# Optimization experiments

Hardware: AMD Instinct MI355X
Metric: run time of the kernel (lower is better)

The kernel has to match this reference:

```python
import jax, jax.numpy as jnp
import numpy as np

# Fixed architecture constants (match init_kwargs)
D_MODEL = 256
NHEAD = 8
BASE_WINDOW = 4
DFF = 1024
B = 1
S = 4096


def _win_idx(grid, w):
    """Token indices of overlapping w x w windows over a grid x grid image,
    stride w//2 (same windows as F.unfold(kernel=w, stride=w//2)). -> (L, w*w) int32."""
    s = w // 2
    starts = np.arange(0, grid - w + 1, s)
    rows = starts[:, None] + np.arange(w)[None, :]              # (n, w)
    idx = rows[:, None, :, None] * grid + rows[None, :, None, :]  # (n, n, w, w)
    return jnp.asarray(idx.reshape(-1, w * w), dtype=jnp.int32)


def _ln(x, g, b, eps=1e-5):
    m = jnp.mean(x, axis=-1, keepdims=True)
    v = jnp.var(x, axis=-1, keepdims=True)
    return (x - m) * jax.lax.rsqrt(v + eps) * g + b


def _local_attn(x, scale, fw, fb, fg, fbb):
    """Multi-scale windowed SDPA: gather windows, attend, mean-pool per window,
    scatter pooled features back to token positions (overlap-averaged), fuse."""
    Bq, Sq, Dm = x.shape
    grid = int(np.sqrt(Sq))
    inv_scale = 1.0 / float(np.sqrt(Dm))  # SDPA uses full D as head dim
    outs = []
    for i in range(3):
        w = BASE_WINDOW * (2 ** i) * scale
        idx = _win_idx(grid, w)                      # (L, w2)
        win = x[:, idx, :]                           # (B, L, w2, D) gather
        p = jax.nn.softmax(jnp.einsum('blqd,blkd->blqk', win, win) * inv_scale, axis=-1)
        pooled = jnp.einsum('blqk,blkd->blqd', p, win).mean(axis=2)  # (B, L, D)
        flat = idx.reshape(-1)
        contrib = jnp.broadcast_to(pooled[:, :, None, :], win.shape).reshape(Bq, -1, Dm)
        acc = jnp.zeros_like(x).at[:, flat, :].add(contrib)
        cnt = jnp.zeros((Sq,), x.dtype).at[flat].add(1.0)
        outs.append(acc / cnt[None, :, None])        # (B, S, D) per scale
    cat = jnp.concatenate(outs, axis=-1)             # (B, S, 3D)
    return _ln(cat @ fw + fb, fg, fbb)


def _mha(x, wq, wk, wv, bq, bk, bv, wo, bo):
    Bq, Sq, Dm = x.shape
    dh = Dm // NHEAD
    def split(t):
        return t.reshape(Bq, Sq, NHEAD, dh)
    q, k, v = split(x @ wq + bq), split(x @ wk + bk), split(x @ wv + bv)
    p = jax.nn.softmax(jnp.einsum('bqhd,bkhd->bhqk', q, k) * (1.0 / float(np.sqrt(dh))), axis=-1)
    o = jnp.einsum('bhqk,bkhd->bqhd', p, v).reshape(Bq, Sq, Dm)
    return o @ wo + bo


def _forward(x, pos, fw, fb, fg, fbb, wq, wk, wv, bq, bk, bv, wo, bo, gw, gb, w1, b1, w2, b2, n1g, n1b, n2g, n2b, n3g, n3b, local_scale):
    # pos is accepted but unused in the original math (device check only)
    xl = _local_attn(x, local_scale, fw, fb, fg, fbb)
    xl = _ln(x + xl, n1g, n1b)                 # norm1 residual (dropout is identity in eval)
    xg = _mha(xl, wq, wk, wv, bq, bk, bv, wo, bo)
    xg = _ln(xl + xg, n2g, n2b)                # norm2 residual
    gate = jax.nn.softmax(((xl + xg) * 0.5).mean(axis=1, keepdims=True) @ gw + gb, axis=-1)  # (B,1,2)
    alpha, beta = gate[..., 0:1], gate[..., 1:2]
    xf = alpha * xg + beta * xl
    ff = jax.nn.gelu(xf @ w1 + b1, approximate=False) @ w2 + b2
    return _ln(xf + ff, n3g, n3b)


def setup_inputs() -> dict:
    key = jax.random.key(0)
    ks = jax.random.split(key, 12)
    def rn(k, shape, s=0.02):
        return jax.random.normal(k, shape, jnp.float32) * s
    D = D_MODEL
    return {
        'x': jax.random.normal(ks[0], (B, S, D), jnp.float32),
        'pos': jax.random.normal(ks[1], (B, S, 2), jnp.float32),
        'fw': rn(ks[2], (3 * D, D)), 'fb': jnp.zeros((D,), jnp.float32),
        'fg': jnp.ones((D,), jnp.float32), 'fbb': jnp.zeros((D,), jnp.float32),
        'wq': rn(ks[3], (D, D)), 'wk': rn(ks[4], (D, D)), 'wv': rn(ks[5], (D, D)),
        'bq': jnp.zeros((D,), jnp.float32), 'bk': jnp.zeros((D,), jnp.float32), 'bv': jnp.zeros((D,), jnp.float32),
        'wo': rn(ks[6], (D, D)), 'bo': jnp.zeros((D,), jnp.float32),
        'gw': rn(ks[7], (D, 2)), 'gb': jnp.zeros((2,), jnp.float32),
        'w1': rn(ks[8], (D, DFF)), 'b1': jnp.zeros((DFF,), jnp.float32),
        'w2': rn(ks[9], (DFF, D)), 'b2': jnp.zeros((D,), jnp.float32),
        'n1g': jnp.ones((D,), jnp.float32), 'n1b': jnp.zeros((D,), jnp.float32),
        'n2g': jnp.ones((D,), jnp.float32), 'n2b': jnp.zeros((D,), jnp.float32),
        'n3g': jnp.ones((D,), jnp.float32), 'n3b': jnp.zeros((D,), jnp.float32),
        'local_scale': 1,
    }


def reference(x, pos, fw, fb, fg, fbb, wq, wk, wv, bq, bk, bv, wo, bo, gw, gb, w1, b1, w2, b2, n1g, n1b, n2g, n2b, n3g, n3b, local_scale):
    return _forward(x, pos, fw, fb, fg, fbb, wq, wk, wv, bq, bk, bv, wo, bo, gw, gb, w1, b1, w2, b2, n1g, n1b, n2g, n2b, n3g, n3b, local_scale)
```

## Files before the change

### kernel.cpp

```cpp
#include <hip/hip_runtime.h>
#include <hip/hip_bf16.h>
#include <cstdint>
#include <cstddef>


#define DEVFN __device__ __forceinline__

constexpr int S    = 4096;
constexpr int D    = 256;
constexpr int GRID = 64;
constexpr int NH   = 8;
constexpr int DH   = 32;

typedef __attribute__((ext_vector_type(8))) short bf16x8;
typedef __attribute__((ext_vector_type(4))) float f32x4;
typedef __attribute__((ext_vector_type(16))) float f32x16;
typedef __attribute__((ext_vector_type(2))) unsigned int u32x2;

DEVFN float asf(unsigned u) { return __uint_as_float(u); }

DEVFN unsigned short f2bf(float f) {
  unsigned u = __float_as_uint(f);
  u += 0x7fffu + ((u >> 16) & 1u);
  return (unsigned short)(u >> 16);
}
DEVFN float bf2f(unsigned short s) { return __uint_as_float(((unsigned)s) << 16); }

DEVFN unsigned pk2(float a, float b) {
  __hip_bfloat162 h = __float22bfloat162_rn(make_float2(a, b));
  return *(unsigned*)&h;
}

DEVFN bf16x8 pack8(float4 a, float4 b) {
  union { unsigned w[4]; bf16x8 v; } u;
  u.w[0] = pk2(a.x, a.y); u.w[1] = pk2(a.z, a.w);
  u.w[2] = pk2(b.x, b.y); u.w[3] = pk2(b.z, b.w);
  return u.v;
}

DEVFN float ex2(float x) {
#if __has_builtin(__builtin_amdgcn_exp2f)
  return __builtin_amdgcn_exp2f(x);
#else
  return __expf(x * 0.6931471805599453f);
#endif
}

DEVFN float gelu_t(float u) {
  const float y = 0.7978845608028654f * (u + 0.044715f * u * u * u);
  const float e = __expf(2.f * y);
  return 0.5f * u * (2.f - 2.f / (e + 1.f));
}

__global__ __launch_bounds__(256) void k_wt(
    const float* fw, const float* wq, const float* wk, const float* wv,
    const float* wo, const float* w1, const float* w2,
    unsigned short* fwT, unsigned short* wqT, unsigned short* wkT,
    unsigned short* wvT, unsigned short* woT, unsigned short* w1T,
    unsigned short* w2T) {
  __shared__ unsigned short tile[32][36];
  const int bid = blockIdx.x;
  const float* src; unsigned short* dst; int K, N, t;
  if (bid < 192)      { src = fw; dst = fwT; K = 768;  N = 256;  t = bid; }
  else if (bid < 256) { src = wq; dst = wqT; K = 256;  N = 256;  t = bid - 192; }
  else if (bid < 320) { src = wk; dst = wkT; K = 256;  N = 256;  t = bid - 256; }
  else if (bid < 384) { src = wv; dst = wvT; K = 256;  N = 256;  t = bid - 320; }
  else if (bid < 448) { src = wo; dst = woT; K = 256;  N = 256;  t = bid - 384; }
  else if (bid < 704) { src = w1; dst = w1T; K = 256;  N = 1024; t = bid - 448; }
  else                { src = w2; dst = w2T; K = 1024; N = 256;  t = bid - 704; }
  const int nkt = K >> 5;
  const int k0 = (t % nkt) * 32, n0 = (t / nkt) * 32;
  const int i = threadIdx.x >> 3, j4 = threadIdx.x & 7;
  const float4 v = *(const float4*)(src + (size_t)(k0 + i) * N + n0 + j4 * 4);
  *(uint2*)&tile[i][j4 * 4] = make_uint2(pk2(v.x, v.y), pk2(v.z, v.w));
  __syncthreads();
  unsigned o0 = tile[j4 * 4 + 0][i], o1 = tile[j4 * 4 + 1][i];
  unsigned o2 = tile[j4 * 4 + 2][i], o3 = tile[j4 * 4 + 3][i];
  *(uint2*)(dst + (size_t)(n0 + i) * K + k0 + j4 * 4) =
      make_uint2(o0 | (o1 << 16), o2 | (o3 << 16));
}

template <int K, int OUTBF, int ACT>
__global__ __launch_bounds__(64) void k_gemm_m(const unsigned short* __restrict__ Ab,
                                               const unsigned short* __restrict__ WT,
                                               const float* __restrict__ bias,
                                               void* __restrict__ Cout, int N) {
  const int lane = threadIdx.x;
  const int lc = lane & 31, hi = lane >> 5;
  const int m0 = blockIdx.x * 32, n0 = blockIdx.y * 32;
  const unsigned short* ap = Ab + (size_t)(m0 + lc) * K + hi * 8;
  const unsigned short* bp = WT + (size_t)(n0 + lc) * K + hi * 8;
  f32x16 acc0 = {0.f,0.f,0.f,0.f,0.f,0.f,0.f,0.f,0.f,0.f,0.f,0.f,0.f,0.f,0.f,0.f};
  f32x16 acc1 = acc0;
#pragma unroll 8
  for (int k0 = 0; k0 < K; k0 += 32) {
    bf16x8 a0 = *(const bf16x8*)(ap + k0);
    bf16x8 b0 = *(const bf16x8*)(bp + k0);
    bf16x8 a1 = *(const bf16x8*)(ap + k0 + 16);
    bf16x8 b1 = *(const bf16x8*)(bp + k0 + 16);
    acc0 = __builtin_amdgcn_mfma_f32_32x32x16_bf16(a0, b0, acc0, 0, 0, 0);
    acc1 = __builtin_amdgcn_mfma_f32_32x32x16_bf16(a1, b1, acc1, 0, 0, 0);
  }
  const float bv = bias[n0 + lc];
#pragma unroll
  for (int r = 0; r < 16; ++r) {
    const int row = (r & 3) + 8 * (r >> 2) + 4 * hi;
    float v = acc0[r] + acc1[r] + bv;
    if (ACT == 1) v = gelu_t(v);
    if (OUTBF) ((unsigned short*)Cout)[(size_t)(m0 + row) * N + n0 + lc] = f2bf(v);
    else       ((float*)Cout)[(size_t)(m0 + row) * N + n0 + lc] = v;
  }
}

__global__ __launch_bounds__(64) void k_gemm_qkv(const unsigned short* __restrict__ Ab,
                                                 const unsigned short* __restrict__ wqkvT,
                                                 const float* __restrict__ bq,
                                                 const float* __restrict__ bk,
                                                 const float* __restrict__ bv,
                                                 unsigned short* __restrict__ qb,
                                                 unsigned short* __restrict__ kb,
                                                 unsigned short* __restrict__ vb) {
  const int lane = threadIdx.x;
  const int lc = lane & 31, hi = lane >> 5;
  const int m0 = blockIdx.x * 32;
  const int sel = blockIdx.y >> 3, n0 = (blockIdx.y & 7) * 32;
  const unsigned short* WT = wqkvT + (size_t)sel * 256 * 256;
  const float* bias = sel == 0 ? bq : sel == 1 ? bk : bv;
  unsigned short* out = sel == 0 ? qb : sel == 1 ? kb : vb;
  const float oscale = sel == 0 ? 0.25505889254f : 1.f;
  const unsigned short* ap = Ab + (size_t)(m0 + lc) * 256 + hi * 8;
  const unsigned short* bp = WT + (size_t)(n0 + lc) * 256 + hi * 8;
  f32x16 acc0 = {0.f,0.f,0.f,0.f,0.f,0.f,0.f,0.f,0.f,0.f,0.f,0.f,0.f,0.f,0.f,0.f};
  f32x16 acc1 = acc0;
#pragma unroll 8
  for (int k0 = 0; k0 < 256; k0 += 32) {
    bf16x8 a0 = *(const bf16x8*)(ap + k0);
    bf16x8 b0 = *(const bf16x8*)(bp + k0);
    bf16x8 a1 = *(const bf16x8*)(ap + k0 + 16);
    bf16x8 b1 = *(const bf16x8*)(bp + k0 + 16);
    acc0 = __builtin_amdgcn_mfma_f32_32x32x16_bf16(a0, b0, acc0, 0, 0, 0);
    acc1 = __builtin_amdgcn_mfma_f32_32x32x16_bf16(a1, b1, acc1, 0, 0, 0);
  }
  const float bvv = bias[n0 + lc];
#pragma unroll
  for (int r = 0; r < 16; ++r) {
    const int row = (r & 3) + 8 * (r >> 2) + 4 * hi;
    out[(size_t)(m0 + row) * 256 + n0 + lc] = f2bf((acc0[r] + acc1[r] + bvv) * oscale);
  }
}

template <int W, int THREADS>
__global__ __launch_bounds__(THREADS) void k_local_s(const float* __restrict__ x,
                                                     float* __restrict__ pooled, int nS) {
  constexpr int NT  = W * W;
  constexpr int NCT = NT / 16;
  constexpr int LDE = 264;
  __shared__ unsigned short win[NT][LDE];
  __shared__ float a[NT];
  const int tid = threadIdx.x;
  const int wave = tid >> 6, lane = tid & 63;
  const int lr = lane & 15, lg = lane >> 4;
  const int l = blockIdx.x;
  const int row0 = (l / nS) * (W / 2), col0 = (l % nS) * (W / 2);

  for (int e8 = tid; e8 < NT * 32; e8 += THREADS) {
    const int t = e8 >> 5, c8 = (e8 & 31) * 8;
    const float* src = x + ((size_t)((row0 + t / W) * GRID + col0 + (t % W))) * D + c8;
    *(bf16x8*)&win[t][c8] = pack8(*(const float4*)src, *(const float4*)(src + 4));
  }
  if (tid < NT) a[tid] = 0.f;
  __syncthreads();

  bf16x8 af[8];
#pragma unroll
  for (int k2 = 0; k2 < 8; ++k2)
    af[k2] = *(const bf16x8*)&win[wave * 16 + lr][k2 * 32 + lg * 8];

  float m[4], Z[4], Zi[4];
#pragma unroll
  for (int r = 0; r < 4; ++r) { m[r] = -INFINITY; Z[r] = 0.f; }

  for (int ct = 0; ct < NCT; ++ct) {
    f32x4 Ca = {0.f, 0.f, 0.f, 0.f}, Cb = {0.f, 0.f, 0.f, 0.f};
#pragma unroll
    for (int k2 = 0; k2 < 8; k2 += 2) {
      bf16x8 b0 = *(const bf16x8*)&win[ct * 16 + lr][k2 * 32 + lg * 8];
      bf16x8 b1 = *(const bf16x8*)&win[ct * 16 + lr][(k2 + 1) * 32 + lg * 8];
      Ca = __builtin_amdgcn_mfma_f32_16x16x32_bf16(af[k2], b0, Ca, 0, 0, 0);
      Cb = __builtin_amdgcn_mfma_f32_16x16x32_bf16(af[k2 + 1], b1, Cb, 0, 0, 0);
    }
#pragma unroll
    for (int r = 0; r < 4; ++r) {
      const float sv = (Ca[r] + Cb[r]) * 0.0625f;
      const float nm = fmaxf(m[r], sv);
      Z[r] = Z[r] * __expf(m[r] - nm) + __expf(sv - nm);
      m[r] = nm;
    }
  }
#pragma unroll
  for (int r = 0; r < 4; ++r) {
#pragma unroll
    for (int msk = 1; msk <= 8; msk <<= 1) {
      const float om = __shfl_xor(m[r], msk), oz = __shfl_xor(Z[r], msk);
      const float nm = fmaxf(m[r], om);
      Z[r] = Z[r] * __expf(m[r] - nm) + oz * __expf(om - nm);
      m[r] = nm;
    }
    Zi[r] = 1.f / Z[r];
  }

  for (int ct = 0; ct < NCT; ++ct) {
    f32x4 Ca = {0.f, 0.f, 0.f, 0.f}, Cb = {0.f, 0.f, 0.f, 0.f};
#pragma unroll
    for (int k2 = 0; k2 < 8; k2 += 2) {
      bf16x8 b0 = *(const bf16x8*)&win[ct * 16 + lr][k2 * 32 + lg * 8];
      bf16x8 b1 = *(const bf16x8*)&win[ct * 16 + lr][(k2 + 1) * 32 + lg * 8];
      Ca = __builtin_amdgcn_mfma_f32_16x16x32_bf16(af[k2], b0, Ca, 0, 0, 0);
      Cb = __builtin_amdgcn_mfma_f32_16x16x32_bf16(af[k2 + 1], b1, Cb, 0, 0, 0);
    }
    float cs = 0.f;
#pragma unroll
    for (int r = 0; r < 4; ++r)
      cs += __expf((Ca[r] + Cb[r]) * 0.0625f - m[r]) * Zi[r];
    cs += __shfl_xor(cs, 16);
    cs += __shfl_xor(cs, 32);
    if (lg == 0) atomicAdd(&a[ct * 16 + lr], cs);
  }
  __syncthreads();

  for (int d = tid; d < D; d += THREADS) {
    float acc = 0.f;
#pragma unroll 8
    for (int k = 0; k < NT; ++k) acc += a[k] * bf2f(win[k][d]);
    pooled[(size_t)l * D + d] = acc * (1.f / NT);
  }
}

__global__ __launch_bounds__(256, 1) void k_local16(const float* __restrict__ x,
                                                    float* __restrict__ pooled, int nS) {
  constexpr int LDE = 264;
  __shared__ unsigned short win[256][LDE];
  __shared__ float a[256];
  const int tid = threadIdx.x;
  const int wave = tid >> 6, lane = tid & 63;
  const int lc = lane & 31, hi = lane >> 5;
  const int l = blockIdx.x, z = blockIdx.y;
  const int row0 = (l / nS) * 8, col0 = (l % nS) * 8;

  for (int e8 = tid; e8 < 256 * 32; e8 += 256) {
    const int t = e8 >> 5, c8 = (e8 & 31) * 8;
    const float* src = x + ((size_t)((row0 + (t >> 4)) * GRID + col0 + (t & 15))) * D + c8;
    *(bf16x8*)&win[t][c8] = pack8(*(const float4*)src, *(const float4*)(src + 4));
  }
  a[tid] = 0.f;
  __syncthreads();

  const int R0 = (z * 4 + wave) * 32;
  bf16x8 af[16];
#pragma unroll
  for (int k2 = 0; k2 < 16; ++k2)
    af[k2] = *(const bf16x8*)&win[R0 + lc][k2 * 16 + hi * 8];

  float m[16], Z[16], Zi[16];
#pragma unroll
  for (int r = 0; r < 16; ++r) { m[r] = -INFINITY; Z[r] = 0.f; }

  for (int ct = 0; ct < 8; ++ct) {
    f32x16 Ca = {0.f,0.f,0.f,0.f,0.f,0.f,0.f,0.f,0.f,0.f,0.f,0.f,0.f,0.f,0.f,0.f};
    f32x16 Cb = Ca;
#pragma unroll
    for (int k2 = 0; k2 < 16; k2 += 2) {
      bf16x8 b0 = *(const bf16x8*)&win[ct * 32 + lc][k2 * 16 + hi * 8];
      bf16x8 b1 = *(const bf16x8*)&win[ct * 32 + lc][(k2 + 1) * 16 + hi * 8];
      Ca = __builtin_amdgcn_mfma_f32_32x32x16_bf16(af[k2], b0, Ca, 0, 0, 0);
      Cb = __builtin_amdgcn_mfma_f32_32x32x16_bf16(af[k2 + 1], b1, Cb, 0, 0, 0);
    }
#pragma unroll
    for (int r = 0; r < 16; ++r) {
      const float sv = (Ca[r] + Cb[r]) * 0.0625f;
      const float nm = fmaxf(m[r], sv);
      Z[r] = Z[r] * __expf(m[r] - nm) + __expf(sv - nm);
      m[r] = nm;
    }
  }
#pragma unroll
  for (int r = 0; r < 16; ++r) {
#pragma unroll
    for (int msk = 1; msk <= 16; msk <<= 1) {
      const float om = __shfl_xor(m[r], msk), oz = __shfl_xor(Z[r], msk);
      const float nm = fmaxf(m[r], om);
      Z[r] = Z[r] * __expf(m[r] - nm) + oz * __expf(om - nm);
      m[r] = nm;
    }
    Zi[r] = 1.f / Z[r];
  }

  for (int ct = 0; ct < 8; ++ct) {
    f32x16 Ca = {0.f,0.f,0.f,0.f,0.f,0.f,0.f,0.f,0.f,0.f,0.f,0.f,0.f,0.f,0.f,0.f};
    f32x16 Cb = Ca;
#pragma unroll
    for (int k2 = 0; k2 < 16; k2 += 2) {
      bf16x8 b0 = *(const bf16x8*)&win[ct * 32 + lc][k2 * 16 + hi * 8];
      bf16x8 b1 = *(const bf16x8*)&win[ct * 32 + lc][(k2 + 1) * 16 + hi * 8];
      Ca = __builtin_amdgcn_mfma_f32_32x32x16_bf16(af[k2], b0, Ca, 0, 0, 0);
      Cb = __builtin_amdgcn_mfma_f32_32x32x16_bf16(af[k2 + 1], b1, Cb, 0, 0, 0);
    }
    float cs = 0.f;
#pragma unroll
    for (int r = 0; r < 16; ++r)
      cs += __expf((Ca[r] + Cb[r]) * 0.0625f - m[r]) * Zi[r];
    cs += __shfl_xor(cs, 32);
    if (hi == 0) atomicAdd(&a[ct * 32 + lc], cs);
  }
  __syncthreads();

  {
    const int d = tid;
    float acc = 0.f;
#pragma unroll 8
    for (int k = 0; k < 256; ++k) acc += a[k] * bf2f(win[k][d]);
    atomicAdd(&pooled[(size_t)l * D + d], acc * (1.f / 256.f));
  }
}

DEVFN float gatherp(const float* __restrict__ pooled, int r, int c, int W, int s, int nS, int d) {
  int amin = max(0, (r - W + s) / s), amax = min(nS - 1, r / s);
  int bmin = max(0, (c - W + s) / s), bmax = min(nS - 1, c / s);
  float acc = 0.f;
  int cnt = 0;
  for (int a = amin; a <= amax; ++a)
    for (int b = bmin; b <= bmax; ++b) { acc += pooled[(size_t)(a * nS + b) * D + d]; ++cnt; }
  return acc / (float)cnt;
}

__global__ void k_combine(const float* __restrict__ p0, const float* __restrict__ p1,
                          const float* __restrict__ p2, unsigned short* __restrict__ catb) {
  const int t = blockIdx.x, d = threadIdx.x;
  const int r = t >> 6, c = t & 63;
  unsigned short* o = catb + (size_t)t * 768;
  o[d]       = f2bf(gatherp(p0, r, c, 4, 2, 31, d));
  o[256 + d] = f2bf(gatherp(p1, r, c, 8, 4, 15, d));
  o[512 + d] = f2bf(gatherp(p2, r, c, 16, 8, 7, d));
}

DEVFN float2 block_sum2(float a, float b) {
  __shared__ float sb[8];
#pragma unroll
  for (int m = 32; m; m >>= 1) { a += __shfl_xor(a, m); b += __shfl_xor(b, m); }
  const int w = threadIdx.x >> 6;
  __syncthreads();
  if ((threadIdx.x & 63) == 0) { sb[w] = a; sb[4 + w] = b; }
  __syncthreads();
  return make_float2(sb[0] + sb[1] + sb[2] + sb[3], sb[4] + sb[5] + sb[6] + sb[7]);
}

__global__ __launch_bounds__(256) void k_ln(float* __restrict__ out, unsigned short* __restrict__ outb,
                                            const float* __restrict__ a, const float* __restrict__ b,
                                            const float* __restrict__ g, const float* __restrict__ be) {
  const size_t i = (size_t)blockIdx.x * D + threadIdx.x;
  float v = a[i] + (b ? b[i] : 0.f);
  float2 s = block_sum2(v, v * v);
  float mean = s.x * (1.f / D);
  float var = s.y * (1.f / D) - mean * mean;
  const float r = (v - mean) * rsqrtf(var + 1e-5f) * g[threadIdx.x] + be[threadIdx.x];
  out[i] = r;
  if (outb) outb[i] = f2bf(r);
}

__global__ __launch_bounds__(256) void k_ln_fuse(const float* __restrict__ t1,
                                                 const float* __restrict__ x,
                                                 float* __restrict__ xl,
                                                 unsigned short* __restrict__ xlb,
                                                 const float* __restrict__ fg,
                                                 const float* __restrict__ fbb,
                                                 const float* __restrict__ n1g,
                                                 const float* __restrict__ n1b) {
  const size_t i = (size_t)blockIdx.x * D + threadIdx.x;
  const float v1 = t1[i];
  float2 s1 = block_sum2(v1, v1 * v1);
  const float mean1 = s1.x * (1.f / D);
  const float var1 = s1.y * (1.f / D) - mean1 * mean1;
  const float r1 = (v1 - mean1) * rsqrtf(var1 + 1e-5f) * fg[threadIdx.x] + fbb[threadIdx.x];
  const float v2 = x[i] + r1;
  float2 s2 = block_sum2(v2, v2 * v2);
  const float mean2 = s2.x * (1.f / D);
  const float var2 = s2.y * (1.f / D) - mean2 * mean2;
  const float r2 = (v2 - mean2) * rsqrtf(var2 + 1e-5f) * n1g[threadIdx.x] + n1b[threadIdx.x];
  xl[i] = r2;
  xlb[i] = f2bf(r2);
}

__global__ __launch_bounds__(256) void k_flash_mfma(const unsigned short* __restrict__ Qg,
                                                    const unsigned short* __restrict__ Kg,
                                                    const unsigned short* __restrict__ Vg,
                                                    unsigned short* __restrict__ po,
                                                    float* __restrict__ pml) {
  const int h = blockIdx.y, z = blockIdx.z;
  const int tid = threadIdx.x;
  const int wave = tid >> 6, lane = tid & 63;
  const int lr = lane & 15, lg = lane >> 4;
  constexpr int NT2 = 16;

  __shared__ unsigned short Kf[2][64][40];
  __shared__ unsigned short VS[2][2048];

  const int q0 = blockIdx.x * 64 + wave * 16;
  const int kbase = z * 1024;

  const bf16x8 qfrag = *(const bf16x8*)(Qg + (size_t)(q0 + lr) * D + h * DH + lg * 8);

  f32x4 o0 = {0.f, 0.f, 0.f, 0.f}, o1 = {0.f, 0.f, 0.f, 0.f};
  float mrow = -INFINITY, lrow = 0.f;

  const unsigned vsbase0 =
      (unsigned)(unsigned long long)(const void*)&VS[0][0] + (unsigned)(lg * 128 + lr * 2);

  const int key = tid >> 2, c8 = (tid & 3) * 8;
  const int vidx = (c8 >> 4) * 1024 + (key >> 2) * 64 + (key & 3) * 16 + (c8 & 15);
  const unsigned short* kp = Kg + (size_t)(kbase + key) * D + h * DH + c8;
  const unsigned short* vp = Vg + (size_t)(kbase + key) * D + h * DH + c8;
  constexpr int KSTEP = 64 * D;

  {
    bf16x8 k0r = *(const bf16x8*)kp;
    bf16x8 v0r = *(const bf16x8*)vp;
    *(bf16x8*)&Kf[0][key][c8] = k0r;
    *(bf16x8*)&VS[0][vidx] = v0r;
  }
  __syncthreads();

  for (int kt = 0; kt < NT2; ++kt) {
    const int cur = kt & 1;
    const int ktn = (kt + 1 < NT2) ? kt + 1 : kt;
    bf16x8 kreg = *(const bf16x8*)(kp + (size_t)ktn * KSTEP);
    bf16x8 vreg = *(const bf16x8*)(vp + (size_t)ktn * KSTEP);

    f32x4 s[4];
    __builtin_amdgcn_s_setprio(1);
#pragma unroll
    for (int k16 = 0; k16 < 4; ++k16) {
      bf16x8 ka = *(const bf16x8*)&Kf[cur][k16 * 16 + lr][lg * 8];
      f32x4 zc = {0.f, 0.f, 0.f, 0.f};
      s[k16] = __builtin_amdgcn_mfma_f32_16x16x32_bf16(ka, qfrag, zc, 0, 0, 0);
    }
    __builtin_amdgcn_s_setprio(0);

    const unsigned vb = vsbase0 + (unsigned)(cur << 12);
    u32x2 tv000, tv001, tv010, tv011, tv100, tv101, tv110, tv111;
    asm volatile("ds_read_b64_tr_b16 %0, %1 offset:0"    : "=v"(tv000) : "v"(vb));
    asm volatile("ds_read_b64_tr_b16 %0, %1 offset:2048" : "=v"(tv001) : "v"(vb));
    asm volatile("ds_read_b64_tr_b16 %0, %1 offset:512"  : "=v"(tv010) : "v"(vb));
    asm volatile("ds_read_b64_tr_b16 %0, %1 offset:2560" : "=v"(tv011) : "v"(vb));
    asm volatile("ds_read_b64_tr_b16 %0, %1 offset:1024" : "=v"(tv100) : "v"(vb));
    asm volatile("ds_read_b64_tr_b16 %0, %1 offset:3072" : "=v"(tv101) : "v"(vb));
    asm volatile("ds_read_b64_tr_b16 %0, %1 offset:1536" : "=v"(tv110) : "v"(vb));
    asm volatile("ds_read_b64_tr_b16 %0, %1 offset:3584" : "=v"(tv111) : "v"(vb));

    float tm = fmaxf(fmaxf(fmaxf(s[0][0], s[0][1]), fmaxf(s[0][2], s[0][3])),
                     fmaxf(fmaxf(s[1][0], s[1][1]), fmaxf(s[1][2], s[1][3])));
    tm = fmaxf(tm, fmaxf(fmaxf(fmaxf(s[2][0], s[2][1]), fmaxf(s[2][2], s[2][3])),
                         fmaxf(fmaxf(s[3][0], s[3][1]), fmaxf(s[3][2], s[3][3]))));
    const bool skip = __all(tm - mrow <= 11.f);
    if (!skip) {
      float tmm = fmaxf(tm, __shfl_xor(tm, 16));
      tmm = fmaxf(tmm, __shfl_xor(tmm, 32));
      const float nm = fmaxf(mrow, tmm);
      const float cfac = ex2(mrow - nm);
      mrow = nm;
      lrow *= cfac;
#pragma unroll
      for (int r = 0; r < 4; ++r) {
        const float cr = __shfl(cfac, lg * 4 + r);
        o0[r] *= cr; o1[r] *= cr;
      }
    }
#pragma unroll
    for (int k16 = 0; k16 < 4; ++k16)
#pragma unroll
      for (int r = 0; r < 4; ++r) { s[k16][r] = ex2(s[k16][r] - mrow); lrow += s[k16][r]; }

    asm volatile("s_waitcnt lgkmcnt(0)" ::: "memory");
    __builtin_amdgcn_sched_barrier(0);

    union VB { u32x2 u2[2]; bf16x8 b; };
    __builtin_amdgcn_s_setprio(1);
#pragma unroll
    for (int kt2 = 0; kt2 < 2; ++kt2) {
      union { unsigned w[4]; bf16x8 v; } pu;
      pu.w[0] = pk2(s[2 * kt2][0], s[2 * kt2][1]);
      pu.w[1] = pk2(s[2 * kt2][2], s[2 * kt2][3]);
      pu.w[2] = pk2(s[2 * kt2 + 1][0], s[2 * kt2 + 1][1]);
      pu.w[3] = pk2(s[2 * kt2 + 1][2], s[2 * kt2 + 1][3]);
      VB v0f, v1f;
      if (kt2 == 0) { v0f.u2[0] = tv000; v0f.u2[1] = tv010; v1f.u2[0] = tv001; v1f.u2[1] = tv011; }
      else          { v0f.u2[0] = tv100; v0f.u2[1] = tv110; v1f.u2[0] = tv101; v1f.u2[1] = tv111; }
      o0 = __builtin_amdgcn_mfma_f32_16x16x32_bf16(pu.v, v0f.b, o0, 0, 0, 0);
      o1 = __builtin_amdgcn_mfma_f32_16x16x32_bf16(pu.v, v1f.b, o1, 0, 0, 0);
    }
    __builtin_amdgcn_s_setprio(0);

    if (kt + 1 < NT2) {
      *(bf16x8*)&Kf[cur ^ 1][key][c8] = kreg;
      *(bf16x8*)&VS[cur ^ 1][vidx] = vreg;
      __syncthreads();
    }
  }

  lrow += __shfl_xor(lrow, 16);
  lrow += __shfl_xor(lrow, 32);

#pragma unroll
  for (int r = 0; r < 4; ++r) {
    unsigned short* op = po + (size_t)z * S * D + (size_t)(q0 + lg * 4 + r) * D + h * DH + lr;
    op[0]  = f2bf(o0[r]);
    op[16] = f2bf(o1[r]);
  }
  if (lane < 16) {
    float* mlp = pml + ((size_t)(z * NH + h) * S + q0 + lr) * 2;
    mlp[0] = mrow;
    mlp[1] = lrow;
  }
}

__global__ __launch_bounds__(256) void k_fmerge(const unsigned short* __restrict__ po,
                                                const float* __restrict__ pml,
                                                unsigned short* __restrict__ t1b) {
  const int t = blockIdx.x, d = threadIdx.x;
  const int h = d >> 5;
  float m[4], l[4];
  float M = -INFINITY;
#pragma unroll
  for (int z = 0; z < 4; ++z) {
    const float* ml = pml + ((size_t)(z * NH + h) * S + t) * 2;
    m[z] = ml[0]; l[z] = ml[1];
    M = fmaxf(M, m[z]);
  }
  float L = 0.f, acc = 0.f;
#pragma unroll
  for (int z = 0; z < 4; ++z) {
    const float a = ex2(m[z] - M);
    L += l[z] * a;
    acc += bf2f(po[(size_t)z * S * D + (size_t)t * D + d]) * a;
  }
  t1b[(size_t)t * D + d] = f2bf(acc / L);
}

__global__ __launch_bounds__(256) void k_colmean(const float* __restrict__ xl,
                                                 const float* __restrict__ xg,
                                                 float* __restrict__ gbuf) {
  const int j = threadIdx.x;
  const int t0 = blockIdx.x * 64;
  float s = 0.f;
  for (int t = 0; t < 64; ++t) {
    size_t i = (size_t)(t0 + t) * D + j;
    s += xl[i] + xg[i];
  }
  atomicAdd(&gbuf[j], s * 0.5f);
}

__global__ __launch_bounds__(256) void k_gate(float* __restrict__ gbuf,
                                              const float* __restrict__ gw,
                                              const float* __restrict__ gb) {
  const int j = threadIdx.x;
  const float gm = gbuf[j] * (1.f / (float)S);
  float2 s = block_sum2(gm * gw[2 * j], gm * gw[2 * j + 1]);
  if (j == 0) {
    float g0 = s.x + gb[0], g1 = s.y + gb[1];
    float mx = fmaxf(g0, g1);
    float e0 = __expf(g0 - mx), e1 = __expf(g1 - mx);
    gbuf[256] = e0 / (e0 + e1);
    gbuf[257] = e1 / (e0 + e1);
  }
}

__global__ __launch_bounds__(256) void k_xf(const float* __restrict__ xl,
                                            const float* __restrict__ xg,
                                            const float* __restrict__ gbuf,
                                            float* __restrict__ xf,
                                            unsigned short* __restrict__ xfb) {
  const float alpha = gbuf[256], beta = gbuf[257];
  const size_t i = ((size_t)blockIdx.x * 256 + threadIdx.x) * 4;
  float4 a = *(const float4*)(xg + i);
  float4 b = *(const float4*)(xl + i);
  float4 r;
  r.x = alpha * a.x + beta * b.x;
  r.y = alpha * a.y + beta * b.y;
  r.z = alpha * a.z + beta * b.z;
  r.w = alpha * a.w + beta * b.w;
  *(float4*)(xf + i) = r;
  *(uint2*)(xfb + i) = make_uint2(pk2(r.x, r.y), pk2(r.z, r.w));
}

extern "C" void kernel_launch(void* const* d_in, const int* in_sizes, int n_in,
                              void* d_out, int out_size, void* d_ws, size_t ws_size,
                              hipStream_t stream) {
  const float* x   = (const float*)d_in[0];
  const float* fw  = (const float*)d_in[2];
  const float* fb  = (const float*)d_in[3];
  const float* fg  = (const float*)d_in[4];
  const float* fbb = (const float*)d_in[5];
  const float* wq  = (const float*)d_in[6];
  const float* wk  = (const float*)d_in[7];
  const float* wv  = (const float*)d_in[8];
  const float* bq  = (const float*)d_in[9];
  const float* bk  = (const float*)d_in[10];
  const float* bv  = (const float*)d_in[11];
  const float* wo  = (const float*)d_in[12];
  const float* bo  = (const float*)d_in[13];
  const float* gw  = (const float*)d_in[14];
  const float* gb  = (const float*)d_in[15];
  const float* w1  = (const float*)d_in[16];
  const float* b1  = (const float*)d_in[17];
  const float* w2  = (const float*)d_in[18];
  const float* b2  = (const float*)d_in[19];
  const float* n1g = (const float*)d_in[20];
  const float* n1b = (const float*)d_in[21];
  const float* n2g = (const float*)d_in[22];
  const float* n2b = (const float*)d_in[23];
  const float* n3g = (const float*)d_in[24];
  const float* n3b = (const float*)d_in[25];
  float* out = (float*)d_out;

  char* base = (char*)d_ws;
  size_t off = 0;
  auto carve = [&](size_t bytes) { char* p = base + off; off += (bytes + 255) & ~(size_t)255; return p; };
  float* p0 = (float*)carve(961 * 256 * 4);
  float* p1 = (float*)carve(225 * 256 * 4);
  float* p2 = (float*)carve(49 * 256 * 4);
  unsigned short* fwT = (unsigned short*)carve(256 * 768 * 2);
  unsigned short* wqkvT = (unsigned short*)carve(3 * 256 * 256 * 2);
  unsigned short* wqT = wqkvT;
  unsigned short* wkT = wqkvT + 256 * 256;
  unsigned short* wvT = wqkvT + 2 * 256 * 256;
  unsigned short* woT = (unsigned short*)carve(256 * 256 * 2);
  unsigned short* w1T = (unsigned short*)carve(1024 * 256 * 2);
  unsigned short* w2T = (unsigned short*)carve(256 * 1024 * 2);
  char* R = carve(8388608);
  unsigned short* catb = (unsigned short*)R;
  unsigned short* po   = (unsigned short*)R;
  float* xg            = (float*)R;
  unsigned short* hbuf = (unsigned short*)R;
  float* pml = (float*)carve(4 * NH * (size_t)S * 2 * 4);
  unsigned short* qb = (unsigned short*)carve((size_t)S * D * 2);
  unsigned short* kb = (unsigned short*)carve((size_t)S * D * 2);
  unsigned short* vb = (unsigned short*)carve((size_t)S * D * 2);
  float* xf            = (float*)qb;
  unsigned short* xfb  = vb;
  float* t1  = (float*)carve((size_t)S * D * 4);
  float* ffo = t1;
  unsigned short* t1b = (unsigned short*)carve((size_t)S * D * 2);
  float* xl  = (float*)carve((size_t)S * D * 4);
  unsigned short* xlb = (unsigned short*)carve((size_t)S * D * 2);
  float* gbuf = (float*)carve(264 * 4);

  hipMemsetAsync(gbuf, 0, 264 * sizeof(float), stream);
  hipMemsetAsync(p2, 0, 49 * 256 * sizeof(float), stream);

  k_wt<<<dim3(960), dim3(256), 0, stream>>>(fw, wq, wk, wv, wo, w1, w2,
                                            fwT, wqT, wkT, wvT, woT, w1T, w2T);
  k_local_s<4, 64><<<dim3(961), dim3(64), 0, stream>>>(x, p0, 31);
  k_local_s<8, 256><<<dim3(225), dim3(256), 0, stream>>>(x, p1, 15);
  k_local16<<<dim3(49, 2), dim3(256), 0, stream>>>(x, p2, 7);
  k_combine<<<dim3(S), dim3(256), 0, stream>>>(p0, p1, p2, catb);
  k_gemm_m<768, 0, 0><<<dim3(S / 32, 8), dim3(64), 0, stream>>>(catb, fwT, fb, t1, 256);
  k_ln_fuse<<<dim3(S), dim3(256), 0, stream>>>(t1, x, xl, xlb, fg, fbb, n1g, n1b);
  k_gemm_qkv<<<dim3(S / 32, 24), dim3(64), 0, stream>>>(xlb, wqkvT, bq, bk, bv, qb, kb, vb);
  k_flash_mfma<<<dim3(S / 64, NH, 4), dim3(256), 0, stream>>>(qb, kb, vb, po, pml);
  k_fmerge<<<dim3(S), dim3(256), 0, stream>>>(po, pml, t1b);
  k_gemm_m<256, 0, 0><<<dim3(S / 32, 8), dim3(64), 0, stream>>>(t1b, woT, bo, xf, 256);
  k_ln<<<dim3(S), dim3(256), 0, stream>>>(xg, nullptr, xl, xf, n2g, n2b);
  k_colmean<<<dim3(64), dim3(256), 0, stream>>>(xl, xg, gbuf);
  k_gate<<<dim3(1), dim3(256), 0, stream>>>(gbuf, gw, gb);
  k_xf<<<dim3(S * D / 1024), dim3(256), 0, stream>>>(xl, xg, gbuf, xf, xfb);
  k_gemm_m<256, 1, 1><<<dim3(S / 32, 32), dim3(64), 0, stream>>>(xfb, w1T, b1, hbuf, 1024);
  k_gemm_m<1024, 0, 0><<<dim3(S / 32, 8), dim3(64), 0, stream>>>(hbuf, w2T, b2, ffo, 256);
  k_ln<<<dim3(S), dim3(256), 0, stream>>>(out, nullptr, xf, ffo, n3g, n3b);
}
```

Before: 213.7 us.

## Fuse three local-attention scale kernels into one launch and load K fragments directly

Merges the three window-scale local attention kernels into a single kernel whose blocks branch by block index, packing four 4x4 windows per block (one per wave) so the smallest scale runs on 256-thread blocks. The goal is to cut two launches and let all scales share the GPU concurrently. In the flash attention kernel, the K tile is no longer staged through shared memory. Each lane now loads its MFMA K fragments straight from global memory with register prefetch, and the row-sum accumulation is split across four partial sums. The trade-off is more global load traffic for K and a larger combined kernel whose 256x264 shared-memory tile is also allocated by the small-window blocks, which limits occupancy.

```diff
diff --git a/kernel.cpp b/kernel.cpp
--- a/kernel.cpp
+++ b/kernel.cpp
@@ -149,177 +149,250 @@
   }
 }
 
-template <int W, int THREADS>
-__global__ __launch_bounds__(THREADS) void k_local_s(const float* __restrict__ x,
-                                                     float* __restrict__ pooled, int nS) {
-  constexpr int NT  = W * W;
-  constexpr int NCT = NT / 16;
+constexpr int NB4 = 241, NB8 = 225, NB16 = 98;
+
+__global__ __launch_bounds__(256, 1) void k_local_all(const float* __restrict__ x,
+                                                      float* __restrict__ p0,
+                                                      float* __restrict__ p1,
+                                                      float* __restrict__ p2) {
   constexpr int LDE = 264;
-  __shared__ unsigned short win[NT][LDE];
-  __shared__ float a[NT];
+  __shared__ unsigned short win[256][LDE];
+  __shared__ float acc[256];
+  const int bid = blockIdx.x;
   const int tid = threadIdx.x;
   const int wave = tid >> 6, lane = tid & 63;
-  const int lr = lane & 15, lg = lane >> 4;
-  const int l = blockIdx.x;
-  const int row0 = (l / nS) * (W / 2), col0 = (l % nS) * (W / 2);
-
-  for (int e8 = tid; e8 < NT * 32; e8 += THREADS) {
-    const int t = e8 >> 5, c8 = (e8 & 31) * 8;
-    const float* src = x + ((size_t)((row0 + t / W) * GRID + col0 + (t % W))) * D + c8;
-    *(bf16x8*)&win[t][c8] = pack8(*(const float4*)src, *(const float4*)(src + 4));
-  }
-  if (tid < NT) a[tid] = 0.f;
-  __syncthreads();
-
-  bf16x8 af[8];
-#pragma unroll
-  for (int k2 = 0; k2 < 8; ++k2)
-    af[k2] = *(const bf16x8*)&win[wave * 16 + lr][k2 * 32 + lg * 8];
-
-  float m[4], Z[4], Zi[4];
-#pragma unroll
-  for (int r = 0; r < 4; ++r) { m[r] = -INFINITY; Z[r] = 0.f; }
-
-  for (int ct = 0; ct < NCT; ++ct) {
-    f32x4 Ca = {0.f, 0.f, 0.f, 0.f}, Cb = {0.f, 0.f, 0.f, 0.f};
-#pragma unroll
-    for (int k2 = 0; k2 < 8; k2 += 2) {
-      bf16x8 b0 = *(const bf16x8*)&win[ct * 16 + lr][k2 * 32 + lg * 8];
-      bf16x8 b1 = *(const bf16x8*)&win[ct * 16 + lr][(k2 + 1) * 32 + lg * 8];
-      Ca = __builtin_amdgcn_mfma_f32_16x16x32_bf16(af[k2], b0, Ca, 0, 0, 0);
-      Cb = __builtin_amdgcn_mfma_f32_16x16x32_bf16(af[k2 + 1], b1, Cb, 0, 0, 0);
+
+  if (bid < NB4) {
+    constexpr int nS = 31;
+    const int widx = bid * 4 + wave;
+    if (widx < 961) {
+      const int lr = lane & 15, lg = lane >> 4;
+      const int row0 = (widx / nS) * 2, col0 = (widx % nS) * 2;
+      unsigned short(*w4)[LDE] = &win[wave * 16];
+      float* a4 = &acc[wave * 16];
+      for (int e8 = lane; e8 < 16 * 32; e8 += 64) {
+        const int t = e8 >> 5, c8 = (e8 & 31) * 8;
+        const float* src = x + ((size_t)((row0 + (t >> 2)) * GRID + col0 + (t & 3))) * D + c8;
+        *(bf16x8*)&w4[t][c8] = pack8(*(const float4*)src, *(const float4*)(src + 4));
+      }
+      if (lane < 16) a4[lane] = 0.f;
+      asm volatile("s_waitcnt lgkmcnt(0)" ::: "memory");
+
+      bf16x8 af[8];
+#pragma unroll
+      for (int k2 = 0; k2 < 8; ++k2)
+        af[k2] = *(const bf16x8*)&w4[lr][k2 * 32 + lg * 8];
+
+      float m[4], Z[4], Zi[4];
+#pragma unroll
+      for (int r = 0; r < 4; ++r) { m[r] = -INFINITY; Z[r] = 0.f; }
+      {
+        f32x4 Ca = {0.f, 0.f, 0.f, 0.f}, Cb = {0.f, 0.f, 0.f, 0.f};
+#pragma unroll
+        for (int k2 = 0; k2 < 8; k2 += 2) {
+          bf16x8 b0 = *(const bf16x8*)&w4[lr][k2 * 32 + lg * 8];
+          bf16x8 b1 = *(const bf16x8*)&w4[lr][(k2 + 1) * 32 + lg * 8];
+          Ca = __builtin_amdgcn_mfma_f32_16x16x32_bf16(af[k2], b0, Ca, 0, 0, 0);
+          Cb = __builtin_amdgcn_mfma_f32_16x16x32_bf16(af[k2 + 1], b1, Cb, 0, 0, 0);
+        }
+#pragma unroll
+        for (int r = 0; r < 4; ++r) {
+          const float sv = (Ca[r] + Cb[r]) * 0.0625f;
+          const float nm = fmaxf(m[r], sv);
+          Z[r] = Z[r] * __expf(m[r] - nm) + __expf(sv - nm);
+          m[r] = nm;
+        }
+      }
+#pragma unroll
+      for (int r = 0; r < 4; ++r) {
+#pragma unroll
+        for (int msk = 1; msk <= 8; msk <<= 1) {
+          const float om = __shfl_xor(m[r], msk), oz = __shfl_xor(Z[r], msk);
+          const float nm = fmaxf(m[r], om);
+          Z[r] = Z[r] * __expf(m[r] - nm) + oz * __expf(om - nm);
+          m[r] = nm;
+        }
+        Zi[r] = 1.f / Z[r];
+      }
+      {
+        f32x4 Ca = {0.f, 0.f, 0.f, 0.f}, Cb = {0.f, 0.f, 0.f, 0.f};
+#pragma unroll
+        for (int k2 = 0; k2 < 8; k2 += 2) {
+          bf16x8 b0 = *(const bf16x8*)&w4[lr][k2 * 32 + lg * 8];
+          bf16x8 b1 = *(const bf16x8*)&w4[lr][(k2 + 1) * 32 + lg * 8];
+          Ca = __builtin_amdgcn_mfma_f32_16x16x32_bf16(af[k2], b0, Ca, 0, 0, 0);
+          Cb = __builtin_amdgcn_mfma_f32_16x16x32_bf16(af[k2 + 1], b1, Cb, 0, 0, 0);
+        }
+        float cs = 0.f;
+#pragma unroll
+        for (int r = 0; r < 4; ++r)
+          cs += __expf((Ca[r] + Cb[r]) * 0.0625f - m[r]) * Zi[r];
+        cs += __shfl_xor(cs, 16);
+        cs += __shfl_xor(cs, 32);
+        if (lg == 0) atomicAdd(&a4[lr], cs);
+      }
+      asm volatile("s_waitcnt lgkmcnt(0)" ::: "memory");
+      for (int d = lane; d < D; d += 64) {
+        float s = 0.f;
+#pragma unroll
+        for (int k = 0; k < 16; ++k) s += a4[k] * bf2f(w4[k][d]);
+        p0[(size_t)widx * D + d] = s * (1.f / 16.f);
+      }
+    }
+  } else if (bid < NB4 + NB8) {
+    constexpr int nS = 15;
+    const int l = bid - NB4;
+    const int lr = lane & 15, lg = lane >> 4;
+    const int row0 = (l / nS) * 4, col0 = (l % nS) * 4;
+    for (int e8 = tid; e8 < 64 * 32; e8 += 256) {
+      const int t = e8 >> 5, c8 = (e8 & 31) * 8;
+      const float* src = x + ((size_t)((row0 + (t >> 3)) * GRID + col0 + (t & 7))) * D + c8;
+      *(bf16x8*)&win[t][c8] = pack8(*(const float4*)src, *(const float4*)(src + 4));
+    }
+    if (tid < 64) acc[tid] = 0.f;
+    __syncthreads();
+
+    bf16x8 af[8];
+#pragma unroll
+    for (int k2 = 0; k2 < 8; ++k2)
+      af[k2] = *(const bf16x8*)&win[wave * 16 + lr][k2 * 32 + lg * 8];
+
+    float m[4], Z[4], Zi[4];
+#pragma unroll
+    for (int r = 0; r < 4; ++r) { m[r] = -INFINITY; Z[r] = 0.f; }
+    for (int ct = 0; ct < 4; ++ct) {
+      f32x4 Ca = {0.f, 0.f, 0.f, 0.f}, Cb = {0.f, 0.f, 0.f, 0.f};
+#pragma unroll
+      for (int k2 = 0; k2 < 8; k2 += 2) {
+        bf16x8 b0 = *(const bf16x8*)&win[ct * 16 + lr][k2 * 32 + lg * 8];
+        bf16x8 b1 = *(const bf16x8*)&win[ct * 16 + lr][(k2 + 1) * 32 + lg * 8];
+        Ca = __builtin_amdgcn_mfma_f32_16x16x32_bf16(af[k2], b0, Ca, 0, 0, 0);
+        Cb = __builtin_amdgcn_mfma_f32_16x16x32_bf16(af[k2 + 1], b1, Cb, 0, 0, 0);
+      }
+#pragma unroll
+      for (int r = 0; r < 4; ++r) {
+        const float sv = (Ca[r] + Cb[r]) * 0.0625f;
+        const float nm = fmaxf(m[r], sv);
+        Z[r] = Z[r] * __expf(m[r] - nm) + __expf(sv - nm);
+        m[r] = nm;
+      }
     }
 #pragma unroll
     for (int r = 0; r < 4; ++r) {
-      const float sv = (Ca[r] + Cb[r]) * 0.0625f;
-      const float nm = fmaxf(m[r], sv);
-      Z[r] = Z[r] * __expf(m[r] - nm) + __expf(sv - nm);
-      m[r] = nm;
-    }
-  }
-#pragma unroll
-  for (int r = 0; r < 4; ++r) {
-#pragma unroll
-    for (int msk = 1; msk <= 8; msk <<= 1) {
-      const float om = __shfl_xor(m[r], msk), oz = __shfl_xor(Z[r], msk);
-      const float nm = fmaxf(m[r], om);
-      Z[r] = Z[r] * __expf(m[r] - nm) + oz * __expf(om - nm);
-      m[r] = nm;
-    }
-    Zi[r] = 1.f / Z[r];
-  }
-
-  for (int ct = 0; ct < NCT; ++ct) {
-    f32x4 Ca = {0.f, 0.f, 0.f, 0.f}, Cb = {0.f, 0.f, 0.f, 0.f};
-#pragma unroll
-    for (int k2 = 0; k2 < 8; k2 += 2) {
-      bf16x8 b0 = *(const bf16x8*)&win[ct * 16 + lr][k2 * 32 + lg * 8];
-      bf16x8 b1 = *(const bf16x8*)&win[ct * 16 + lr][(k2 + 1) * 32 + lg * 8];
-      Ca = __builtin_amdgcn_mfma_f32_16x16x32_bf16(af[k2], b0, Ca, 0, 0, 0);
-      Cb = __builtin_amdgcn_mfma_f32_16x16x32_bf16(af[k2 + 1], b1, Cb, 0, 0, 0);
-    }
-    float cs = 0.f;
-#pragma unroll
-    for (int r = 0; r < 4; ++r)
-      cs += __expf((Ca[r] + Cb[r]) * 0.0625f - m[r]) * Zi[r];
-    cs += __shfl_xor(cs, 16);
-    cs += __shfl_xor(cs, 32);
-    if (lg == 0) atomicAdd(&a[ct * 16 + lr], cs);
-  }
-  __syncthreads();
-
-  for (int d = tid; d < D; d += THREADS) {
-    float acc = 0.f;
+#pragma unroll
+      for (int msk = 1; msk <= 8; msk <<= 1) {
+        const float om = __shfl_xor(m[r], msk), oz = __shfl_xor(Z[r], msk);
+        const float nm = fmaxf(m[r], om);
+        Z[r] = Z[r] * __expf(m[r] - nm) + oz * __expf(om - nm);
+        m[r] = nm;
+      }
+      Zi[r] = 1.f / Z[r];
+    }
+    for (int ct = 0; ct < 4; ++ct) {
+      f32x4 Ca = {0.f, 0.f, 0.f, 0.f}, Cb = {0.f, 0.f, 0.f, 0.f};
+#pragma unroll
+      for (int k2 = 0; k2 < 8; k2 += 2) {
+        bf16x8 b0 = *(const bf16x8*)&win[ct * 16 + lr][k2 * 32 + lg * 8];
+        bf16x8 b1 = *(const bf16x8*)&win[ct * 16 + lr][(k2 + 1) * 32 + lg * 8];
+        Ca = __builtin_amdgcn_mfma_f32_16x16x32_bf16(af[k2], b0, Ca, 0, 0, 0);
+        Cb = __builtin_amdgcn_mfma_f32_16x16x32_bf16(af[k2 + 1], b1, Cb, 0, 0, 0);
+      }
+      float cs = 0.f;
+#pragma unroll
+      for (int r = 0; r < 4; ++r)
+        cs += __expf((Ca[r] + Cb[r]) * 0.0625f - m[r]) * Zi[r];
+      cs += __shfl_xor(cs, 16);
+      cs += __shfl_xor(cs, 32);
+      if (lg == 0) atomicAdd(&acc[ct * 16 + lr], cs);
+    }
+    __syncthreads();
+    {
+      const int d = tid;
+      float s = 0.f;
 #pragma unroll 8
-    for (int k = 0; k < NT; ++k) acc += a[k] * bf2f(win[k][d]);
-    pooled[(size_t)l * D + d] = acc * (1.f / NT);
-  }
-}
-
-__global__ __launch_bounds__(256, 1) void k_local16(const float* __restrict__ x,
-                                                    float* __restrict__ pooled, int nS) {
-  constexpr int LDE = 264;
-  __shared__ unsigned short win[256][LDE];
-  __shared__ float a[256];
-  const int tid = threadIdx.x;
-  const int wave = tid >> 6, lane = tid & 63;
-  const int lc = lane & 31, hi = lane >> 5;
-  const int l = blockIdx.x, z = blockIdx.y;
-  const int row0 = (l / nS) * 8, col0 = (l % nS) * 8;
-
-  for (int e8 = tid; e8 < 256 * 32; e8 += 256) {
-    const int t = e8 >> 5, c8 = (e8 & 31) * 8;
-    const float* src = x + ((size_t)((row0 + (t >> 4)) * GRID + col0 + (t & 15))) * D + c8;
-    *(bf16x8*)&win[t][c8] = pack8(*(const float4*)src, *(const float4*)(src + 4));
-  }
-  a[tid] = 0.f;
-  __syncthreads();
-
-  const int R0 = (z * 4 + wave) * 32;
-  bf16x8 af[16];
-#pragma unroll
-  for (int k2 = 0; k2 < 16; ++k2)
-    af[k2] = *(const bf16x8*)&win[R0 + lc][k2 * 16 + hi * 8];
-
-  float m[16], Z[16], Zi[16];
-#pragma unroll
-  for (int r = 0; r < 16; ++r) { m[r] = -INFINITY; Z[r] = 0.f; }
-
-  for (int ct = 0; ct < 8; ++ct) {
-    f32x16 Ca = {0.f,0.f,0.f,0.f,0.f,0.f,0.f,0.f,0.f,0.f,0.f,0.f,0.f,0.f,0.f,0.f};
-    f32x16 Cb = Ca;
-#pragma unroll
-    for (int k2 = 0; k2 < 16; k2 += 2) {
-      bf16x8 b0 = *(const bf16x8*)&win[ct * 32 + lc][k2 * 16 + hi * 8];
-      bf16x8 b1 = *(const bf16x8*)&win[ct * 32 + lc][(k2 + 1) * 16 + hi * 8];
-      Ca = __builtin_amdgcn_mfma_f32_32x32x16_bf16(af[k2], b0, Ca, 0, 0, 0);
-      Cb = __builtin_amdgcn_mfma_f32_32x32x16_bf16(af[k2 + 1], b1, Cb, 0, 0, 0);
+      for (int k = 0; k < 64; ++k) s += acc[k] * bf2f(win[k][d]);
+      p1[(size_t)l * D + d] = s * (1.f / 64.f);
+    }
+  } else {
+    constexpr int nS = 7;
+    const int zz = bid - NB4 - NB8;
+    const int l = zz >> 1, z = zz & 1;
+    const int lc = lane & 31, hi = lane >> 5;
+    const int row0 = (l / nS) * 8, col0 = (l % nS) * 8;
+
+    for (int e8 = tid; e8 < 256 * 32; e8 += 256) {
+      const int t = e8 >> 5, c8 = (e8 & 31) * 8;
+      const float* src = x + ((size_t)((row0 + (t >> 4)) * GRID + col0 + (t & 15))) * D + c8;
+      *(bf16x8*)&win[t][c8] = pack8(*(const float4*)src, *(const float4*)(src + 4));
+    }
+    acc[tid] = 0.f;
+    __syncthreads();
+
+    const int R0 = (z * 4 + wave) * 32;
+    bf16x8 af[16];
+#pragma unroll
+    for (int k2 = 0; k2 < 16; ++k2)
+      af[k2] = *(const bf16x8*)&win[R0 + lc][k2 * 16 + hi * 8];
+
+    float m[16], Z[16], Zi[16];
+#pragma unroll
+    for (int r = 0; r < 16; ++r) { m[r] = -INFINITY; Z[r] = 0.f; }
+
+    for (int ct = 0; ct < 8; ++ct) {
+      f32x16 Ca = {0.f,0.f,0.f,0.f,0.f,0.f,0.f,0.f,0.f,0.f,0.f,0.f,0.f,0.f,0.f,0.f};
+      f32x16 Cb = Ca;
+#pragma unroll
+      for (int k2 = 0; k2 < 16; k2 += 2) {
+        bf16x8 b0 = *(const bf16x8*)&win[ct * 32 + lc][k2 * 16 + hi * 8];
+        bf16x8 b1 = *(const bf16x8*)&win[ct * 32 + lc][(k2 + 1) * 16 + hi * 8];
+        Ca = __builtin_amdgcn_mfma_f32_32x32x16_bf16(af[k2], b0, Ca, 0, 0, 0);
+        Cb = __builtin_amdgcn_mfma_f32_32x32x16_bf16(af[k2 + 1], b1, Cb, 0, 0, 0);
+      }
+#pragma unroll
+      for (int r = 0; r < 16; ++r) {
+        const float sv = (Ca[r] + Cb[r]) * 0.0625f;
+        const float nm = fmaxf(m[r], sv);
+        Z[r] = Z[r] * __expf(m[r] - nm) + __expf(sv - nm);
+        m[r] = nm;
+      }
     }
 #pragma unroll
     for (int r = 0; r < 16; ++r) {
-      const float sv = (Ca[r] + Cb[r]) * 0.0625f;
-      const float nm = fmaxf(m[r], sv);
-      Z[r] = Z[r] * __expf(m[r] - nm) + __expf(sv - nm);
-      m[r] = nm;
-    }
-  }
-#pragma unroll
-  for (int r = 0; r < 16; ++r) {
-#pragma unroll
-    for (int msk = 1; msk <= 16; msk <<= 1) {
-      const float om = __shfl_xor(m[r], msk), oz = __shfl_xor(Z[r], msk);
-      const float nm = fmaxf(m[r], om);
-      Z[r] = Z[r] * __expf(m[r] - nm) + oz * __expf(om - nm);
-      m[r] = nm;
-    }
-    Zi[r] = 1.f / Z[r];
-  }
-
-  for (int ct = 0; ct < 8; ++ct) {
-    f32x16 Ca = {0.f,0.f,0.f,0.f,0.f,0.f,0.f,0.f,0.f,0.f,0.f,0.f,0.f,0.f,0.f,0.f};
-    f32x16 Cb = Ca;
-#pragma unroll
-    for (int k2 = 0; k2 < 16; k2 += 2) {
-      bf16x8 b0 = *(const bf16x8*)&win[ct * 32 + lc][k2 * 16 + hi * 8];
-      bf16x8 b1 = *(const bf16x8*)&win[ct * 32 + lc][(k2 + 1) * 16 + hi * 8];
-      Ca = __builtin_amdgcn_mfma_f32_32x32x16_bf16(af[k2], b0, Ca, 0, 0, 0);
-      Cb = __builtin_amdgcn_mfma_f32_32x32x16_bf16(af[k2 + 1], b1, Cb, 0, 0, 0);
-    }
-    float cs = 0.f;
-#pragma unroll
-    for (int r = 0; r < 16; ++r)
-      cs += __expf((Ca[r] + Cb[r]) * 0.0625f - m[r]) * Zi[r];
-    cs += __shfl_xor(cs, 32);
-    if (hi == 0) atomicAdd(&a[ct * 32 + lc], cs);
-  }
-  __syncthreads();
-
-  {
-    const int d = tid;
-    float acc = 0.f;
+#pragma unroll
+      for (int msk = 1; msk <= 16; msk <<= 1) {
+        const float om = __shfl_xor(m[r], msk), oz = __shfl_xor(Z[r], msk);
+        const float nm = fmaxf(m[r], om);
+        Z[r] = Z[r] * __expf(m[r] - nm) + oz * __expf(om - nm);
+        m[r] = nm;
+      }
+      Zi[r] = 1.f / Z[r];
+    }
+
+    for (int ct = 0; ct < 8; ++ct) {
+      f32x16 Ca = {0.f,0.f,0.f,0.f,0.f,0.f,0.f,0.f,0.f,0.f,0.f,0.f,0.f,0.f,0.f,0.f};
+      f32x16 Cb = Ca;
+#pragma unroll
+      for (int k2 = 0; k2 < 16; k2 += 2) {
+        bf16x8 b0 = *(const bf16x8*)&win[ct * 32 + lc][k2 * 16 + hi * 8];
+        bf16x8 b1 = *(const bf16x8*)&win[ct * 32 + lc][(k2 + 1) * 16 + hi * 8];
+        Ca = __builtin_amdgcn_mfma_f32_32x32x16_bf16(af[k2], b0, Ca, 0, 0, 0);
+        Cb = __builtin_amdgcn_mfma_f32_32x32x16_bf16(af[k2 + 1], b1, Cb, 0, 0, 0);
+      }
+      float cs = 0.f;
+#pragma unroll
+      for (int r = 0; r < 16; ++r)
+        cs += __expf((Ca[r] + Cb[r]) * 0.0625f - m[r]) * Zi[r];
+      cs += __shfl_xor(cs, 32);
+      if (hi == 0) atomicAdd(&acc[ct * 32 + lc], cs);
+    }
+    __syncthreads();
+    {
+      const int d = tid;
+      float s = 0.f;
 #pragma unroll 8
-    for (int k = 0; k < 256; ++k) acc += a[k] * bf2f(win[k][d]);
-    atomicAdd(&pooled[(size_t)l * D + d], acc * (1.f / 256.f));
+      for (int k = 0; k < 256; ++k) s += acc[k] * bf2f(win[k][d]);
+      atomicAdd(&p2[(size_t)l * D + d], s * (1.f / 256.f));
+    }
   }
 }
 
@@ -401,7 +474,6 @@
   const int lr = lane & 15, lg = lane >> 4;
   constexpr int NT2 = 16;
 
-  __shared__ unsigned short Kf[2][64][40];
   __shared__ unsigned short VS[2][2048];
 
   const int q0 = blockIdx.x * 64 + wave * 16;
@@ -417,31 +489,38 @@
 
   const int key = tid >> 2, c8 = (tid & 3) * 8;
   const int vidx = (c8 >> 4) * 1024 + (key >> 2) * 64 + (key & 3) * 16 + (c8 & 15);
-  const unsigned short* kp = Kg + (size_t)(kbase + key) * D + h * DH + c8;
   const unsigned short* vp = Vg + (size_t)(kbase + key) * D + h * DH + c8;
+  const unsigned short* kfp = Kg + (size_t)(kbase + lr) * D + h * DH + lg * 8;
   constexpr int KSTEP = 64 * D;
 
   {
-    bf16x8 k0r = *(const bf16x8*)kp;
     bf16x8 v0r = *(const bf16x8*)vp;
-    *(bf16x8*)&Kf[0][key][c8] = k0r;
     *(bf16x8*)&VS[0][vidx] = v0r;
   }
+  bf16x8 kf0 = *(const bf16x8*)(kfp);
+  bf16x8 kf1 = *(const bf16x8*)(kfp + 16 * D);
+  bf16x8 kf2 = *(const bf16x8*)(kfp + 32 * D);
+  bf16x8 kf3 = *(const bf16x8*)(kfp + 48 * D);
   __syncthreads();
 
   for (int kt = 0; kt < NT2; ++kt) {
     const int cur = kt & 1;
     const int ktn = (kt + 1 < NT2) ? kt + 1 : kt;
-    bf16x8 kreg = *(const bf16x8*)(kp + (size_t)ktn * KSTEP);
+    const unsigned short* kfpn = kfp + (size_t)ktn * KSTEP;
+    bf16x8 kn0 = *(const bf16x8*)(kfpn);
+    bf16x8 kn1 = *(const bf16x8*)(kfpn + 16 * D);
+    bf16x8 kn2 = *(const bf16x8*)(kfpn + 32 * D);
+    bf16x8 kn3 = *(const bf16x8*)(kfpn + 48 * D);
     bf16x8 vreg = *(const bf16x8*)(vp + (size_t)ktn * KSTEP);
 
     f32x4 s[4];
     __builtin_amdgcn_s_setprio(1);
-#pragma unroll
-    for (int k16 = 0; k16 < 4; ++k16) {
-      bf16x8 ka = *(const bf16x8*)&Kf[cur][k16 * 16 + lr][lg * 8];
+    {
       f32x4 zc = {0.f, 0.f, 0.f, 0.f};
-      s[k16] = __builtin_amdgcn_mfma_f32_16x16x32_bf16(ka, qfrag, zc, 0, 0, 0);
+      s[0] = __builtin_amdgcn_mfma_f32_16x16x32_bf16(kf0, qfrag, zc, 0, 0, 0);
+      s[1] = __builtin_amdgcn_mfma_f32_16x16x32_bf16(kf1, qfrag, zc, 0, 0, 0);
+      s[2] = __builtin_amdgcn_mfma_f32_16x16x32_bf16(kf2, qfrag, zc, 0, 0, 0);
+      s[3] = __builtin_amdgcn_mfma_f32_16x16x32_bf16(kf3, qfrag, zc, 0, 0, 0);
     }
     __builtin_amdgcn_s_setprio(0);
 
@@ -474,10 +553,15 @@
         o0[r] *= cr; o1[r] *= cr;
       }
     }
-#pragma unroll
-    for (int k16 = 0; k16 < 4; ++k16)
-#pragma unroll
-      for (int r = 0; r < 4; ++r) { s[k16][r] = ex2(s[k16][r] - mrow); lrow += s[k16][r]; }
+    float pa = 0.f, pb = 0.f, pc = 0.f, pd = 0.f;
+#pragma unroll
+    for (int k16 = 0; k16 < 4; ++k16) {
+      s[k16][0] = ex2(s[k16][0] - mrow); pa += s[k16][0];
+      s[k16][1] = ex2(s[k16][1] - mrow); pb += s[k16][1];
+      s[k16][2] = ex2(s[k16][2] - mrow); pc += s[k16][2];
+      s[k16][3] = ex2(s[k16][3] - mrow); pd += s[k16][3];
+    }
+    lrow += (pa + pb) + (pc + pd);
 
     asm volatile("s_waitcnt lgkmcnt(0)" ::: "memory");
     __builtin_amdgcn_sched_barrier(0);
@@ -500,10 +584,10 @@
     __builtin_amdgcn_s_setprio(0);
 
     if (kt + 1 < NT2) {
-      *(bf16x8*)&Kf[cur ^ 1][key][c8] = kreg;
       *(bf16x8*)&VS[cur ^ 1][vidx] = vreg;
       __syncthreads();
     }
+    kf0 = kn0; kf1 = kn1; kf2 = kn2; kf3 = kn3;
   }
 
   lrow += __shfl_xor(lrow, 16);
@@ -658,9 +742,7 @@
 
   k_wt<<<dim3(960), dim3(256), 0, stream>>>(fw, wq, wk, wv, wo, w1, w2,
                                             fwT, wqT, wkT, wvT, woT, w1T, w2T);
-  k_local_s<4, 64><<<dim3(961), dim3(64), 0, stream>>>(x, p0, 31);
-  k_local_s<8, 256><<<dim3(225), dim3(256), 0, stream>>>(x, p1, 15);
-  k_local16<<<dim3(49, 2), dim3(256), 0, stream>>>(x, p2, 7);
+  k_local_all<<<dim3(NB4 + NB8 + NB16), dim3(256), 0, stream>>>(x, p0, p1, p2);
   k_combine<<<dim3(S), dim3(256), 0, stream>>>(p0, p1, p2, catb);
   k_gemm_m<768, 0, 0><<<dim3(S / 32, 8), dim3(64), 0, stream>>>(catb, fwT, fb, t1, 256);
   k_ln_fuse<<<dim3(S), dim3(256), 0, stream>>>(t1, x, xl, xlb, fg, fbb, n1g, n1b);
```

After: 235.2 us. 10.1% more time.
